# Kernel optimization log

Hardware: AMD Instinct MI355X
Metric: run time of the kernel (lower is better)

Reference implementation:

```python
import jax, jax.numpy as jnp
import numpy as np

D_MODEL = 1024
NUM_HEADS = 16
D_K = D_MODEL // NUM_HEADS
B, T = 2, 2048
NEG = -1e9


def setup_inputs() -> dict:
    key = jax.random.key(0)
    ks = jax.random.split(key, 12)
    s = 1.0 / np.sqrt(D_MODEL)
    q = jax.random.normal(ks[0], (B, T, D_MODEL), jnp.float32)
    k = jax.random.normal(ks[1], (B, T, D_MODEL), jnp.float32)
    v = jax.random.normal(ks[2], (B, T, D_MODEL), jnp.float32)
    # padding mask: True = valid key; realistic per-example lengths
    lengths = jnp.array([T, 3 * T // 4], dtype=jnp.int32)
    key_padding_mask = jnp.arange(T)[None, :] < lengths[:, None]
    Wq = jax.random.uniform(ks[3], (D_MODEL, D_MODEL), jnp.float32, -s, s)
    bq = jax.random.uniform(ks[4], (D_MODEL,), jnp.float32, -s, s)
    Wk = jax.random.uniform(ks[5], (D_MODEL, D_MODEL), jnp.float32, -s, s)
    bk = jax.random.uniform(ks[6], (D_MODEL,), jnp.float32, -s, s)
    Wv = jax.random.uniform(ks[7], (D_MODEL, D_MODEL), jnp.float32, -s, s)
    bv = jax.random.uniform(ks[8], (D_MODEL,), jnp.float32, -s, s)
    Wo = jax.random.uniform(ks[9], (D_MODEL, D_MODEL), jnp.float32, -s, s)
    bo = jax.random.uniform(ks[10], (D_MODEL,), jnp.float32, -s, s)
    return {"q": q, "k": k, "v": v, "key_padding_mask": key_padding_mask,
            "Wq": Wq, "bq": bq, "Wk": Wk, "bk": bk,
            "Wv": Wv, "bv": bv, "Wo": Wo, "bo": bo}


def reference(q, k, v, key_padding_mask, Wq, bq, Wk, bk, Wv, bv, Wo, bo):
    Bq, Tq, D = q.shape
    Tk = k.shape[1]
    # projections (torch Linear: x @ W.T + b), split heads -> [B, H, T, d_k]
    Q = (q @ Wq.T + bq).reshape(Bq, Tq, NUM_HEADS, D_K).transpose(0, 2, 1, 3)
    K = (k @ Wk.T + bk).reshape(Bq, Tk, NUM_HEADS, D_K).transpose(0, 2, 1, 3)
    V = (v @ Wv.T + bv).reshape(Bq, Tk, NUM_HEADS, D_K).transpose(0, 2, 1, 3)
    logits = jnp.einsum("bhqd,bhkd->bhqk", Q, K) / jnp.sqrt(jnp.float32(D_K))
    causal = jnp.tril(jnp.ones((Tq, Tk), dtype=bool))  # [Tq, Tk]
    mask = causal[None, None, :, :] & key_padding_mask[:, None, None, :]
    logits = jnp.where(mask, logits, NEG)
    scores = jax.nn.softmax(logits, axis=-1)
    out = jnp.einsum("bhqk,bhkd->bhqd", scores, V)
    out = out.transpose(0, 2, 1, 3).reshape(Bq, Tq, D)
    # dropout is identity in eval mode
    return out @ Wo.T + bo
```

## Files before the change

### kernel.cpp

```cpp
#include <hip/hip_runtime.h>
#include <stdint.h>

#define D_MODEL 1024
#define NHEAD 16
#define DK 64
#define BATCH 2
#define SEQ 2048
#define NROW 4096

typedef __attribute__((ext_vector_type(8))) _Float16 f16x8;
typedef __attribute__((ext_vector_type(4))) float f32x4;

__device__ __forceinline__ uint16_t f2h(float x) {
    _Float16 h = (_Float16)x;
    union { _Float16 h; uint16_t u; } cv;
    cv.h = h;
    return cv.u;
}

__device__ __forceinline__ float fexp2(float x) {
#if __has_builtin(__builtin_amdgcn_exp2f)
    return __builtin_amdgcn_exp2f(x);
#else
    return exp2f(x);
#endif
}

__device__ __forceinline__ void lds_dma16(const uint16_t* g, uint16_t* l) {
    __builtin_amdgcn_global_load_lds((const __attribute__((address_space(1))) void*)g,
                                     (__attribute__((address_space(3))) void*)l,
                                     16, 0, 0);
}

struct CvtArgs {
    const float* src[7];
    uint16_t* dst[7];
    int n4[7];
};
__global__ void cvt_all_kernel(CvtArgs a, const int* __restrict__ mask, int* __restrict__ lens) {
    int t = blockIdx.y;
    if (t == 7) {
        if (blockIdx.x != 0) return;
        __shared__ int red[256];
        int tid = threadIdx.x;
        int mx = 0;
        for (int i = tid; i < 1024; i += 256) { int v = mask[i]; if (v > mx) mx = v; }
        red[tid] = mx; __syncthreads();
        for (int s = 128; s > 0; s >>= 1) { if (tid < s) { if (red[tid+s] > red[tid]) red[tid] = red[tid+s]; } __syncthreads(); }
        int bytemode = (red[0] > 1);
        __syncthreads();
        const unsigned char* mb = (const unsigned char*)mask;
        for (int b = 0; b < BATCH; ++b) {
            int cnt = 0;
            for (int tt = tid; tt < SEQ; tt += 256) {
                int v = bytemode ? (int)mb[b*SEQ + tt] : mask[b*SEQ + tt];
                cnt += (v != 0) ? 1 : 0;
            }
            red[tid] = cnt; __syncthreads();
            for (int s = 128; s > 0; s >>= 1) { if (tid < s) red[tid] += red[tid+s]; __syncthreads(); }
            if (tid == 0) lens[b] = red[0];
            __syncthreads();
        }
        return;
    }
    const float* src = a.src[t];
    uint16_t* dst = a.dst[t];
    int n4 = a.n4[t];
    int i = blockIdx.x * blockDim.x + threadIdx.x;
    int stride = gridDim.x * blockDim.x;
    for (; i < n4; i += stride) {
        float4 v = ((const float4*)src)[i];
        ushort4 o;
        o.x = f2h(v.x); o.y = f2h(v.y); o.z = f2h(v.z); o.w = f2h(v.w);
        ((ushort4*)dst)[i] = o;
    }
}

__device__ __forceinline__ void gemm_tile_core(const uint16_t* __restrict__ A,
                                               const uint16_t* __restrict__ W,
                                               int bx, int by,
                                               uint16_t* As, uint16_t* Bs,
                                               f32x4 (&acc)[4][4]) {
    const f32x4 fzero = {0.f, 0.f, 0.f, 0.f};
    int tid = threadIdx.x;
    int lane = tid & 63, wave = tid >> 6;
    int wm = wave >> 1, wn = wave & 1;
    int l15 = lane & 15, quad = lane >> 4;
    int rl = lane >> 3, cb8 = lane & 7;
#pragma unroll
    for (int mi = 0; mi < 4; mi++)
#pragma unroll
        for (int ni = 0; ni < 4; ni++) acc[mi][ni] = fzero;

    for (int k0 = 0; k0 < D_MODEL; k0 += 64) {
        __syncthreads();
#pragma unroll
        for (int i = 0; i < 4; ++i) {
            int d8 = wave * 4 + i;
            int row = d8 * 8 + rl;
            int cbg = cb8 ^ rl;
            lds_dma16(A + (size_t)(bx * 128 + row) * D_MODEL + k0 + cbg * 8, As + d8 * 512);
            lds_dma16(W + (size_t)(by * 128 + row) * D_MODEL + k0 + cbg * 8, Bs + d8 * 512);
        }
        __syncthreads();
#pragma unroll
        for (int ks = 0; ks < 2; ks++) {
            f16x8 af[4], bf[4];
#pragma unroll
            for (int mi = 0; mi < 4; mi++) {
                int row = wm * 64 + mi * 16 + l15;
                af[mi] = *(const f16x8*)(As + row * 64 + (((ks * 4 + quad) ^ (row & 7)) * 8));
            }
#pragma unroll
            for (int ni = 0; ni < 4; ni++) {
                int row = wn * 64 + ni * 16 + l15;
                bf[ni] = *(const f16x8*)(Bs + row * 64 + (((ks * 4 + quad) ^ (row & 7)) * 8));
            }
#pragma unroll
            for (int mi = 0; mi < 4; mi++)
#pragma unroll
                for (int ni = 0; ni < 4; ni++)
                    acc[mi][ni] = __builtin_amdgcn_mfma_f32_16x16x32_f16(af[mi], bf[ni], acc[mi][ni], 0, 0, 0);
        }
    }
}

#define TS_STRIDE 136
__global__ __launch_bounds__(256, 3) void qkv_kernel(
    const uint16_t* __restrict__ qb, const uint16_t* __restrict__ kb, const uint16_t* __restrict__ vb,
    const uint16_t* __restrict__ wq, const uint16_t* __restrict__ wk, const uint16_t* __restrict__ wv,
    const float* __restrict__ bq, const float* __restrict__ bk, const float* __restrict__ bv,
    uint16_t* __restrict__ Qh, uint16_t* __restrict__ Kh, uint16_t* __restrict__ Vth) {
    __shared__ uint16_t smem[TS_STRIDE * 128];
    uint16_t* As = smem;
    uint16_t* Bs = smem + 128 * 64;
    int v = blockIdx.z;
    const uint16_t* A = (v == 0) ? qb : ((v == 1) ? kb : vb);
    const uint16_t* W = (v == 0) ? wq : ((v == 1) ? wk : wv);
    const float* bias = (v == 0) ? bq : ((v == 1) ? bk : bv);
    f32x4 acc[4][4];
    gemm_tile_core(A, W, blockIdx.x, blockIdx.y, As, Bs, acc);

    int tid = threadIdx.x, lane = tid & 63, wave = tid >> 6;
    int wm = wave >> 1, wn = wave & 1, l15 = lane & 15, quad = lane >> 4;
    const float QSCALE = 0.125f * 1.44269504088896f;

    if (v == 2) {
        __syncthreads();
        uint16_t* Ts = smem;
#pragma unroll
        for (int mi = 0; mi < 4; mi++) {
#pragma unroll
            for (int ni = 0; ni < 4; ni++) {
                int col = wn * 64 + ni * 16 + l15;
                float bcol = bias[blockIdx.y * 128 + col];
#pragma unroll
                for (int r = 0; r < 4; r++) {
                    int tl = wm * 64 + mi * 16 + quad * 4 + r;
                    Ts[col * TS_STRIDE + tl] = f2h(acc[mi][ni][r] + bcol);
                }
            }
        }
        __syncthreads();
        int col = tid >> 1, th = (tid & 1) << 6;
        int gcol = blockIdx.y * 128 + col;
        int h = gcol >> 6, d = gcol & 63;
        int grow0 = blockIdx.x * 128;
        int b = grow0 >> 11, t = (grow0 & (SEQ - 1)) + th;
        size_t base = (((size_t)(b * NHEAD + h) << 6) + d) * SEQ + t;
#pragma unroll
        for (int j = 0; j < 8; j++)
            *(uint4*)(Vth + base + j * 8) = *(const uint4*)(Ts + col * TS_STRIDE + th + j * 8);
        return;
    }

#pragma unroll
    for (int mi = 0; mi < 4; mi++) {
#pragma unroll
        for (int ni = 0; ni < 4; ni++) {
            int gcol = blockIdx.y * 128 + wn * 64 + ni * 16 + l15;
            float bcol = bias[gcol];
            int h = gcol >> 6, d = gcol & 63;
#pragma unroll
            for (int r = 0; r < 4; r++) {
                int grow = blockIdx.x * 128 + wm * 64 + mi * 16 + quad * 4 + r;
                int b = grow >> 11, t = grow & (SEQ - 1);
                float val = acc[mi][ni][r] + bcol;
                size_t bh = (size_t)(b * NHEAD + h);
                if (v == 0) Qh[(bh * SEQ + t) * 64 + d] = f2h(val * QSCALE);
                else        Kh[(bh * SEQ + t) * 64 + d] = f2h(val);
            }
        }
    }
}

__global__ __launch_bounds__(256, 3) void outproj_kernel(
    const uint16_t* __restrict__ attn, const uint16_t* __restrict__ wo,
    const float* __restrict__ bo, float* __restrict__ out) {
    __shared__ uint16_t As[128 * 64], Bs[128 * 64];
    f32x4 acc[4][4];
    gemm_tile_core(attn, wo, blockIdx.x, blockIdx.y, As, Bs, acc);
    int tid = threadIdx.x, lane = tid & 63, wave = tid >> 6;
    int wm = wave >> 1, wn = wave & 1, l15 = lane & 15, quad = lane >> 4;
#pragma unroll
    for (int mi = 0; mi < 4; mi++) {
#pragma unroll
        for (int ni = 0; ni < 4; ni++) {
            int gcol = blockIdx.y * 128 + wn * 64 + ni * 16 + l15;
            float bcol = bo[gcol];
#pragma unroll
            for (int r = 0; r < 4; r++) {
                int grow = blockIdx.x * 128 + wm * 64 + mi * 16 + quad * 4 + r;
                out[(size_t)grow * D_MODEL + gcol] = acc[mi][ni][r] + bcol;
            }
        }
    }
}

#define PIPE_WAIT2_BARRIER() do { asm volatile("s_waitcnt vmcnt(2)" ::: "memory"); __builtin_amdgcn_s_barrier(); } while (0)
#define PIPE_WAIT0_BARRIER() do { asm volatile("s_waitcnt vmcnt(0)" ::: "memory"); __builtin_amdgcn_s_barrier(); } while (0)

__device__ __forceinline__ void flash_item(
    int qt, int bh, int b, int h, int L,
    const uint16_t* __restrict__ Qh, const uint16_t* __restrict__ Kh, const uint16_t* __restrict__ Vth,
    uint16_t* __restrict__ attn,
    uint16_t* KtA, uint16_t* VtA, uint16_t* Ptw) {
    const f32x4 fzero = {0.f, 0.f, 0.f, 0.f};
    const float MFIX = 6.0f;
    int tid = threadIdx.x, lane = tid & 63, w = tid >> 6;
    int l15 = lane & 15, quad = lane >> 4, l7 = l15 & 7;
    int q0 = qt * 64;
    int rl = lane >> 3, cb8 = lane & 7;

    f16x8 ones;
#pragma unroll
    for (int j = 0; j < 8; j++) ones[j] = (_Float16)1.0f;

    f16x8 qf[2];
#pragma unroll
    for (int ks = 0; ks < 2; ks++)
        qf[ks] = *(const f16x8*)(Qh + ((size_t)bh * SEQ + q0 + w * 16 + l15) * 64 + ks * 32 + quad * 8);

    f32x4 o_acc[4], l_acc = fzero;
#pragma unroll
    for (int ni = 0; ni < 4; ni++) o_acc[ni] = fzero;

    int nkt_p = (L + 63) >> 6;
    int nkt = (qt + 1 < nkt_p) ? (qt + 1) : nkt_p;

    const uint16_t* Kbh = Kh + (size_t)bh * SEQ * 64;
    const uint16_t* Vbh = Vth + ((size_t)bh << 6) * SEQ;

    auto stageK = [&](int kt_, int slot) {
#pragma unroll
        for (int i_ = 0; i_ < 2; ++i_) {
            int d8 = w * 2 + i_;
            int row = d8 * 8 + rl;
            int cbg = cb8 ^ rl;
            lds_dma16(Kbh + (size_t)(kt_ * 64 + row) * 64 + cbg * 8, KtA + slot * 4096 + d8 * 512);
        }
    };
    auto stageV = [&](int kt_, int slot) {
#pragma unroll
        for (int i_ = 0; i_ < 2; ++i_) {
            int d8 = w * 2 + i_;
            int row = d8 * 8 + rl;
            int cbg = cb8 ^ rl;
            lds_dma16(Vbh + (size_t)row * SEQ + kt_ * 64 + cbg * 8, VtA + slot * 4096 + d8 * 512);
        }
    };

    stageV(0, 0);
    stageK(0, 0);
    PIPE_WAIT0_BARRIER();
    stageK((1 < nkt) ? 1 : 0, 1);

    int kcur = 0, vcur = 0;
    for (int kt = 0; kt < nkt; ++kt) {
        int ktV = (kt + 1 < nkt) ? kt + 1 : nkt - 1;
        int ktK = (kt + 2 < nkt) ? kt + 2 : nkt - 1;
        stageV(ktV, (kt + 1) & 1);
        int ks2 = (kcur >= 1) ? kcur - 1 : 2;
        stageK(ktK, ks2);

        const uint16_t* Kc = KtA + kcur * 4096;
        const uint16_t* Vc = VtA + vcur * 4096;

        f32x4 s_acc[4];
#pragma unroll
        for (int ni = 0; ni < 4; ni++) s_acc[ni] = fzero;
#pragma unroll
        for (int ks = 0; ks < 2; ks++) {
            f16x8 kf[4];
#pragma unroll
            for (int ni = 0; ni < 4; ni++) {
                int row = ni * 16 + l15;
                kf[ni] = *(const f16x8*)(Kc + row * 64 + (((ks * 4 + quad) ^ (row & 7)) * 8));
            }
#pragma unroll
            for (int ni = 0; ni < 4; ni++)
                s_acc[ni] = __builtin_amdgcn_mfma_f32_16x16x32_f16(qf[ks], kf[ni], s_acc[ni], 0, 0, 0);
        }

        bool full = (kt < qt) && (kt * 64 + 64 <= L);
#pragma unroll
        for (int r = 0; r < 4; r++) {
            int prow = quad * 4 + r;
            int q_idx = q0 + w * 16 + prow;
            int pr7 = prow & 7;
#pragma unroll
            for (int ni = 0; ni < 4; ni++) {
                float s = s_acc[ni][r];
                if (!full) {
                    int key = kt * 64 + ni * 16 + l15;
                    s = ((key <= q_idx) && (key < L)) ? s : -1e9f;
                }
                float p = fexp2(s - MFIX);
                int cb = ni * 2 + (l15 >> 3);
                Ptw[prow * 64 + ((cb ^ pr7) * 8) + l7] = f2h(p);
            }
        }
        __asm__ __volatile__("" ::: "memory");

#pragma unroll
        for (int ks = 0; ks < 2; ks++) {
            f16x8 pa = *(const f16x8*)(Ptw + l15 * 64 + (((ks * 4 + quad) ^ l7) * 8));
            l_acc = __builtin_amdgcn_mfma_f32_16x16x32_f16(pa, ones, l_acc, 0, 0, 0);
            f16x8 vbf[4];
#pragma unroll
            for (int ni = 0; ni < 4; ni++) {
                int row = ni * 16 + l15;
                vbf[ni] = *(const f16x8*)(Vc + row * 64 + (((ks * 4 + quad) ^ (row & 7)) * 8));
            }
#pragma unroll
            for (int ni = 0; ni < 4; ni++)
                o_acc[ni] = __builtin_amdgcn_mfma_f32_16x16x32_f16(pa, vbf[ni], o_acc[ni], 0, 0, 0);
        }

        PIPE_WAIT2_BARRIER();
        kcur = (kcur == 2) ? 0 : kcur + 1;
        vcur ^= 1;
    }

#pragma unroll
    for (int r = 0; r < 4; r++) {
        float inv = 1.0f / l_acc[r];
        int q_idx = q0 + w * 16 + quad * 4 + r;
#pragma unroll
        for (int ni = 0; ni < 4; ni++) {
            attn[((size_t)(b * SEQ + q_idx)) * D_MODEL + h * 64 + ni * 16 + l15] =
                f2h(o_acc[ni][r] * inv);
        }
    }
}

__global__ __launch_bounds__(256, 3) void attn_kernel(
    const uint16_t* __restrict__ Qh, const uint16_t* __restrict__ Kh, const uint16_t* __restrict__ Vth,
    uint16_t* __restrict__ attn, const int* __restrict__ lens) {
    __shared__ uint16_t Kt[3 * 4096];
    __shared__ uint16_t Vt[2 * 4096];
    __shared__ uint16_t Pt[4 * 1024];
    int n = (int)blockIdx.x;
    int xcd = n & 7;
    int i = n >> 3;
    int j = (xcd << 2) | (i & 3);
    int bh = ((j & 1) << 4) | (j >> 1);
    int x = i >> 2;
    int b = bh >> 4, h = bh & 15;
    int L = lens[b];
    int w = threadIdx.x >> 6;
    uint16_t* Ptw = Pt + w * 1024;
    flash_item(31 - x, bh, b, h, L, Qh, Kh, Vth, attn, Kt, Vt, Ptw);
    flash_item(x, bh, b, h, L, Qh, Kh, Vth, attn, Kt, Vt, Ptw);
}

extern "C" void kernel_launch(void* const* d_in, const int* in_sizes, int n_in,
                              void* d_out, int out_size, void* d_ws, size_t ws_size,
                              hipStream_t stream) {
    const float* q  = (const float*)d_in[0];
    const float* k  = (const float*)d_in[1];
    const float* v  = (const float*)d_in[2];
    const int*   mask = (const int*)d_in[3];
    const float* Wq = (const float*)d_in[4];
    const float* bq = (const float*)d_in[5];
    const float* Wk = (const float*)d_in[6];
    const float* bk = (const float*)d_in[7];
    const float* Wv = (const float*)d_in[8];
    const float* bv = (const float*)d_in[9];
    const float* Wo = (const float*)d_in[10];
    const float* bo = (const float*)d_in[11];
    float* out = (float*)d_out;

    char* ws = (char*)d_ws;
    size_t off = 0;
    auto alloc = [&](size_t bytes) -> char* {
        char* p = ws + off;
        off += (bytes + 255) & ~(size_t)255;
        return p;
    };
    const size_t inp_e = (size_t)NROW * D_MODEL;
    const size_t w_e   = (size_t)D_MODEL * D_MODEL;
    uint16_t* qbf  = (uint16_t*)alloc(inp_e * 2);
    uint16_t* kbf  = (uint16_t*)alloc(inp_e * 2);
    uint16_t* vbf  = (uint16_t*)alloc(inp_e * 2);
    uint16_t* wqb  = (uint16_t*)alloc(w_e * 2);
    uint16_t* wkb  = (uint16_t*)alloc(w_e * 2);
    uint16_t* wvb  = (uint16_t*)alloc(w_e * 2);
    uint16_t* wob  = (uint16_t*)alloc(w_e * 2);
    uint16_t* Qhb  = (uint16_t*)alloc(inp_e * 2);
    uint16_t* Khb  = (uint16_t*)alloc(inp_e * 2);
    uint16_t* Vtb  = (uint16_t*)alloc(inp_e * 2);
    uint16_t* attb = (uint16_t*)alloc(inp_e * 2);
    int* lens      = (int*)alloc(256);

    CvtArgs ca;
    ca.src[0] = q;  ca.dst[0] = qbf; ca.n4[0] = (int)(inp_e / 4);
    ca.src[1] = k;  ca.dst[1] = kbf; ca.n4[1] = (int)(inp_e / 4);
    ca.src[2] = v;  ca.dst[2] = vbf; ca.n4[2] = (int)(inp_e / 4);
    ca.src[3] = Wq; ca.dst[3] = wqb; ca.n4[3] = (int)(w_e / 4);
    ca.src[4] = Wk; ca.dst[4] = wkb; ca.n4[4] = (int)(w_e / 4);
    ca.src[5] = Wv; ca.dst[5] = wvb; ca.n4[5] = (int)(w_e / 4);
    ca.src[6] = Wo; ca.dst[6] = wob; ca.n4[6] = (int)(w_e / 4);
    cvt_all_kernel<<<dim3(128, 8), 256, 0, stream>>>(ca, mask, lens);

    qkv_kernel<<<dim3(32, 8, 3), 256, 0, stream>>>(qbf, kbf, vbf, wqb, wkb, wvb,
                                                   bq, bk, bv, Qhb, Khb, Vtb);
    attn_kernel<<<dim3(512, 1), 256, 0, stream>>>(Qhb, Khb, Vtb, attb, lens);
    outproj_kernel<<<dim3(32, 8), 256, 0, stream>>>(attb, wob, bo, out);
}
```

Before: 227.6 us.

## Process paired causal query tiles in one pass sharing K/V tile loads

Each block now processes its two query tiles (a long one, 31-x, and a short one, x) together in a single KV loop rather than two sequential loops. The short tile reuses each staged K/V tile while it is active, which cuts repeated global-to-LDS staging and pipeline restarts. The change also adds s_setprio around the MFMA sections, doubles the P scratch, and reorders block-to-tile mapping. In exchange, register use rises and occupancy is dropped from 3 to 2 blocks per CU.

```diff
diff --git a/kernel.cpp b/kernel.cpp
--- a/kernel.cpp
+++ b/kernel.cpp
@@ -220,33 +220,36 @@
 #define PIPE_WAIT2_BARRIER() do { asm volatile("s_waitcnt vmcnt(2)" ::: "memory"); __builtin_amdgcn_s_barrier(); } while (0)
 #define PIPE_WAIT0_BARRIER() do { asm volatile("s_waitcnt vmcnt(0)" ::: "memory"); __builtin_amdgcn_s_barrier(); } while (0)
 
-__device__ __forceinline__ void flash_item(
-    int qt, int bh, int b, int h, int L,
+__device__ __forceinline__ void flash_pair(
+    int qtA, int qtB, int bh, int b, int h, int L,
     const uint16_t* __restrict__ Qh, const uint16_t* __restrict__ Kh, const uint16_t* __restrict__ Vth,
     uint16_t* __restrict__ attn,
-    uint16_t* KtA, uint16_t* VtA, uint16_t* Ptw) {
+    uint16_t* KtA, uint16_t* VtA, uint16_t* PtwA, uint16_t* PtwB) {
     const f32x4 fzero = {0.f, 0.f, 0.f, 0.f};
     const float MFIX = 6.0f;
     int tid = threadIdx.x, lane = tid & 63, w = tid >> 6;
     int l15 = lane & 15, quad = lane >> 4, l7 = l15 & 7;
-    int q0 = qt * 64;
+    int q0A = qtA * 64, q0B = qtB * 64;
     int rl = lane >> 3, cb8 = lane & 7;
 
     f16x8 ones;
 #pragma unroll
     for (int j = 0; j < 8; j++) ones[j] = (_Float16)1.0f;
 
-    f16x8 qf[2];
-#pragma unroll
-    for (int ks = 0; ks < 2; ks++)
-        qf[ks] = *(const f16x8*)(Qh + ((size_t)bh * SEQ + q0 + w * 16 + l15) * 64 + ks * 32 + quad * 8);
-
-    f32x4 o_acc[4], l_acc = fzero;
-#pragma unroll
-    for (int ni = 0; ni < 4; ni++) o_acc[ni] = fzero;
+    f16x8 qfA[2], qfB[2];
+#pragma unroll
+    for (int ks = 0; ks < 2; ks++) {
+        qfA[ks] = *(const f16x8*)(Qh + ((size_t)bh * SEQ + q0A + w * 16 + l15) * 64 + ks * 32 + quad * 8);
+        qfB[ks] = *(const f16x8*)(Qh + ((size_t)bh * SEQ + q0B + w * 16 + l15) * 64 + ks * 32 + quad * 8);
+    }
+
+    f32x4 oA[4], oB[4], lAcc = fzero, lBcc = fzero;
+#pragma unroll
+    for (int ni = 0; ni < 4; ni++) { oA[ni] = fzero; oB[ni] = fzero; }
 
     int nkt_p = (L + 63) >> 6;
-    int nkt = (qt + 1 < nkt_p) ? (qt + 1) : nkt_p;
+    int nktA = (qtA + 1 < nkt_p) ? (qtA + 1) : nkt_p;
+    int nktB = (qtB + 1 < nkt_p) ? (qtB + 1) : nkt_p;
 
     const uint16_t* Kbh = Kh + (size_t)bh * SEQ * 64;
     const uint16_t* Vbh = Vth + ((size_t)bh << 6) * SEQ;
@@ -273,22 +276,24 @@
     stageV(0, 0);
     stageK(0, 0);
     PIPE_WAIT0_BARRIER();
-    stageK((1 < nkt) ? 1 : 0, 1);
+    stageK((1 < nktA) ? 1 : 0, 1);
 
     int kcur = 0, vcur = 0;
-    for (int kt = 0; kt < nkt; ++kt) {
-        int ktV = (kt + 1 < nkt) ? kt + 1 : nkt - 1;
-        int ktK = (kt + 2 < nkt) ? kt + 2 : nkt - 1;
+    for (int kt = 0; kt < nktA; ++kt) {
+        int ktV = (kt + 1 < nktA) ? kt + 1 : nktA - 1;
+        int ktK = (kt + 2 < nktA) ? kt + 2 : nktA - 1;
         stageV(ktV, (kt + 1) & 1);
         int ks2 = (kcur >= 1) ? kcur - 1 : 2;
         stageK(ktK, ks2);
 
         const uint16_t* Kc = KtA + kcur * 4096;
         const uint16_t* Vc = VtA + vcur * 4096;
-
-        f32x4 s_acc[4];
-#pragma unroll
-        for (int ni = 0; ni < 4; ni++) s_acc[ni] = fzero;
+        bool actB = (kt < nktB);
+
+        f32x4 sA[4], sB[4];
+#pragma unroll
+        for (int ni = 0; ni < 4; ni++) { sA[ni] = fzero; sB[ni] = fzero; }
+        __builtin_amdgcn_s_setprio(1);
 #pragma unroll
         for (int ks = 0; ks < 2; ks++) {
             f16x8 kf[4];
@@ -299,33 +304,67 @@
             }
 #pragma unroll
             for (int ni = 0; ni < 4; ni++)
-                s_acc[ni] = __builtin_amdgcn_mfma_f32_16x16x32_f16(qf[ks], kf[ni], s_acc[ni], 0, 0, 0);
-        }
-
-        bool full = (kt < qt) && (kt * 64 + 64 <= L);
-#pragma unroll
-        for (int r = 0; r < 4; r++) {
-            int prow = quad * 4 + r;
-            int q_idx = q0 + w * 16 + prow;
-            int pr7 = prow & 7;
-#pragma unroll
-            for (int ni = 0; ni < 4; ni++) {
-                float s = s_acc[ni][r];
-                if (!full) {
-                    int key = kt * 64 + ni * 16 + l15;
-                    s = ((key <= q_idx) && (key < L)) ? s : -1e9f;
+                sA[ni] = __builtin_amdgcn_mfma_f32_16x16x32_f16(qfA[ks], kf[ni], sA[ni], 0, 0, 0);
+            if (actB) {
+#pragma unroll
+                for (int ni = 0; ni < 4; ni++)
+                    sB[ni] = __builtin_amdgcn_mfma_f32_16x16x32_f16(qfB[ks], kf[ni], sB[ni], 0, 0, 0);
+            }
+        }
+        __builtin_amdgcn_s_setprio(0);
+
+        {
+            bool fullA = (kt < qtA) && (kt * 64 + 64 <= L);
+#pragma unroll
+            for (int r = 0; r < 4; r++) {
+                int prow = quad * 4 + r;
+                int q_idx = q0A + w * 16 + prow;
+                int pr7 = prow & 7;
+#pragma unroll
+                for (int ni = 0; ni < 4; ni++) {
+                    float s = sA[ni][r];
+                    if (!fullA) {
+                        int key = kt * 64 + ni * 16 + l15;
+                        s = ((key <= q_idx) && (key < L)) ? s : -1e9f;
+                    }
+                    float p = fexp2(s - MFIX);
+                    int cb = ni * 2 + (l15 >> 3);
+                    PtwA[prow * 64 + ((cb ^ pr7) * 8) + l7] = f2h(p);
                 }
-                float p = fexp2(s - MFIX);
-                int cb = ni * 2 + (l15 >> 3);
-                Ptw[prow * 64 + ((cb ^ pr7) * 8) + l7] = f2h(p);
+            }
+        }
+        if (actB) {
+            bool fullB = (kt < qtB) && (kt * 64 + 64 <= L);
+#pragma unroll
+            for (int r = 0; r < 4; r++) {
+                int prow = quad * 4 + r;
+                int q_idx = q0B + w * 16 + prow;
+                int pr7 = prow & 7;
+#pragma unroll
+                for (int ni = 0; ni < 4; ni++) {
+                    float s = sB[ni][r];
+                    if (!fullB) {
+                        int key = kt * 64 + ni * 16 + l15;
+                        s = ((key <= q_idx) && (key < L)) ? s : -1e9f;
+                    }
+                    float p = fexp2(s - MFIX);
+                    int cb = ni * 2 + (l15 >> 3);
+                    PtwB[prow * 64 + ((cb ^ pr7) * 8) + l7] = f2h(p);
+                }
             }
         }
         __asm__ __volatile__("" ::: "memory");
 
+        __builtin_amdgcn_s_setprio(1);
 #pragma unroll
         for (int ks = 0; ks < 2; ks++) {
-            f16x8 pa = *(const f16x8*)(Ptw + l15 * 64 + (((ks * 4 + quad) ^ l7) * 8));
-            l_acc = __builtin_amdgcn_mfma_f32_16x16x32_f16(pa, ones, l_acc, 0, 0, 0);
+            f16x8 paA = *(const f16x8*)(PtwA + l15 * 64 + (((ks * 4 + quad) ^ l7) * 8));
+            lAcc = __builtin_amdgcn_mfma_f32_16x16x32_f16(paA, ones, lAcc, 0, 0, 0);
+            f16x8 paB;
+            if (actB) {
+                paB = *(const f16x8*)(PtwB + l15 * 64 + (((ks * 4 + quad) ^ l7) * 8));
+                lBcc = __builtin_amdgcn_mfma_f32_16x16x32_f16(paB, ones, lBcc, 0, 0, 0);
+            }
             f16x8 vbf[4];
 #pragma unroll
             for (int ni = 0; ni < 4; ni++) {
@@ -334,8 +373,14 @@
             }
 #pragma unroll
             for (int ni = 0; ni < 4; ni++)
-                o_acc[ni] = __builtin_amdgcn_mfma_f32_16x16x32_f16(pa, vbf[ni], o_acc[ni], 0, 0, 0);
-        }
+                oA[ni] = __builtin_amdgcn_mfma_f32_16x16x32_f16(paA, vbf[ni], oA[ni], 0, 0, 0);
+            if (actB) {
+#pragma unroll
+                for (int ni = 0; ni < 4; ni++)
+                    oB[ni] = __builtin_amdgcn_mfma_f32_16x16x32_f16(paB, vbf[ni], oB[ni], 0, 0, 0);
+            }
+        }
+        __builtin_amdgcn_s_setprio(0);
 
         PIPE_WAIT2_BARRIER();
         kcur = (kcur == 2) ? 0 : kcur + 1;
@@ -344,34 +389,46 @@
 
 #pragma unroll
     for (int r = 0; r < 4; r++) {
-        float inv = 1.0f / l_acc[r];
-        int q_idx = q0 + w * 16 + quad * 4 + r;
+        float inv = 1.0f / lAcc[r];
+        int q_idx = q0A + w * 16 + quad * 4 + r;
 #pragma unroll
         for (int ni = 0; ni < 4; ni++) {
             attn[((size_t)(b * SEQ + q_idx)) * D_MODEL + h * 64 + ni * 16 + l15] =
-                f2h(o_acc[ni][r] * inv);
-        }
-    }
-}
-
-__global__ __launch_bounds__(256, 3) void attn_kernel(
+                f2h(oA[ni][r] * inv);
+        }
+    }
+#pragma unroll
+    for (int r = 0; r < 4; r++) {
+        float inv = 1.0f / lBcc[r];
+        int q_idx = q0B + w * 16 + quad * 4 + r;
+#pragma unroll
+        for (int ni = 0; ni < 4; ni++) {
+            attn[((size_t)(b * SEQ + q_idx)) * D_MODEL + h * 64 + ni * 16 + l15] =
+                f2h(oB[ni][r] * inv);
+        }
+    }
+}
+
+__global__ __launch_bounds__(256, 2) void attn_kernel(
     const uint16_t* __restrict__ Qh, const uint16_t* __restrict__ Kh, const uint16_t* __restrict__ Vth,
     uint16_t* __restrict__ attn, const int* __restrict__ lens) {
     __shared__ uint16_t Kt[3 * 4096];
     __shared__ uint16_t Vt[2 * 4096];
-    __shared__ uint16_t Pt[4 * 1024];
+    __shared__ uint16_t Pt[8 * 1024];
     int n = (int)blockIdx.x;
     int xcd = n & 7;
     int i = n >> 3;
-    int j = (xcd << 2) | (i & 3);
-    int bh = ((j & 1) << 4) | (j >> 1);
-    int x = i >> 2;
+    int hs = i & 3;
+    int j = i >> 2;
+    int x = (j < 8) ? j : (23 - j);
+    int jj = (xcd << 2) | hs;
+    int bh = ((jj & 1) << 4) | (jj >> 1);
     int b = bh >> 4, h = bh & 15;
     int L = lens[b];
     int w = threadIdx.x >> 6;
-    uint16_t* Ptw = Pt + w * 1024;
-    flash_item(31 - x, bh, b, h, L, Qh, Kh, Vth, attn, Kt, Vt, Ptw);
-    flash_item(x, bh, b, h, L, Qh, Kh, Vth, attn, Kt, Vt, Ptw);
+    uint16_t* PtwA = Pt + w * 2048;
+    uint16_t* PtwB = PtwA + 1024;
+    flash_pair(31 - x, x, bh, b, h, L, Qh, Kh, Vth, attn, Kt, Vt, PtwA, PtwB);
 }
 
 extern "C" void kernel_launch(void* const* d_in, const int* in_sizes, int n_in,
```

Result: slower. 235.2 us (+3.3%).

## Load K/V fragments directly from global memory, dropping LDS staging pipeline

Applied to the files above, without the earlier changes.

The attention kernel no longer stages K and V tiles into shared memory through async LDS DMA with a triple/double-buffered pipeline and barriers. Each wave now reads its MFMA K and V fragments straight from global memory into registers at the start of every key tile, so the block-wide barriers and most of the LDS footprint go away. The cost is that the four waves each fetch the same K/V data redundantly through L1/L2, with no prefetch overlap across iterations. Launch bounds are lowered from 3 to 2 blocks per SM to leave room for the extra registers.

```diff
diff --git a/kernel.cpp b/kernel.cpp
--- a/kernel.cpp
+++ b/kernel.cpp
@@ -217,20 +217,15 @@
     }
 }
 
-#define PIPE_WAIT2_BARRIER() do { asm volatile("s_waitcnt vmcnt(2)" ::: "memory"); __builtin_amdgcn_s_barrier(); } while (0)
-#define PIPE_WAIT0_BARRIER() do { asm volatile("s_waitcnt vmcnt(0)" ::: "memory"); __builtin_amdgcn_s_barrier(); } while (0)
-
 __device__ __forceinline__ void flash_item(
     int qt, int bh, int b, int h, int L,
     const uint16_t* __restrict__ Qh, const uint16_t* __restrict__ Kh, const uint16_t* __restrict__ Vth,
-    uint16_t* __restrict__ attn,
-    uint16_t* KtA, uint16_t* VtA, uint16_t* Ptw) {
+    uint16_t* __restrict__ attn, uint16_t* Ptw) {
     const f32x4 fzero = {0.f, 0.f, 0.f, 0.f};
     const float MFIX = 6.0f;
     int tid = threadIdx.x, lane = tid & 63, w = tid >> 6;
     int l15 = lane & 15, quad = lane >> 4, l7 = l15 & 7;
     int q0 = qt * 64;
-    int rl = lane >> 3, cb8 = lane & 7;
 
     f16x8 ones;
 #pragma unroll
@@ -248,59 +243,34 @@
     int nkt_p = (L + 63) >> 6;
     int nkt = (qt + 1 < nkt_p) ? (qt + 1) : nkt_p;
 
-    const uint16_t* Kbh = Kh + (size_t)bh * SEQ * 64;
+    const uint16_t* kb = Kh + (size_t)bh * SEQ * 64 + l15 * 64 + quad * 8;
     const uint16_t* Vbh = Vth + ((size_t)bh << 6) * SEQ;
-
-    auto stageK = [&](int kt_, int slot) {
-#pragma unroll
-        for (int i_ = 0; i_ < 2; ++i_) {
-            int d8 = w * 2 + i_;
-            int row = d8 * 8 + rl;
-            int cbg = cb8 ^ rl;
-            lds_dma16(Kbh + (size_t)(kt_ * 64 + row) * 64 + cbg * 8, KtA + slot * 4096 + d8 * 512);
-        }
-    };
-    auto stageV = [&](int kt_, int slot) {
-#pragma unroll
-        for (int i_ = 0; i_ < 2; ++i_) {
-            int d8 = w * 2 + i_;
-            int row = d8 * 8 + rl;
-            int cbg = cb8 ^ rl;
-            lds_dma16(Vbh + (size_t)row * SEQ + kt_ * 64 + cbg * 8, VtA + slot * 4096 + d8 * 512);
-        }
-    };
-
-    stageV(0, 0);
-    stageK(0, 0);
-    PIPE_WAIT0_BARRIER();
-    stageK((1 < nkt) ? 1 : 0, 1);
-
-    int kcur = 0, vcur = 0;
+    const uint16_t* vb0 = Vbh + (size_t)(l15) * SEQ + quad * 8;
+    const uint16_t* vb1 = Vbh + (size_t)(16 + l15) * SEQ + quad * 8;
+    const uint16_t* vb2 = Vbh + (size_t)(32 + l15) * SEQ + quad * 8;
+    const uint16_t* vb3 = Vbh + (size_t)(48 + l15) * SEQ + quad * 8;
+
     for (int kt = 0; kt < nkt; ++kt) {
-        int ktV = (kt + 1 < nkt) ? kt + 1 : nkt - 1;
-        int ktK = (kt + 2 < nkt) ? kt + 2 : nkt - 1;
-        stageV(ktV, (kt + 1) & 1);
-        int ks2 = (kcur >= 1) ? kcur - 1 : 2;
-        stageK(ktK, ks2);
-
-        const uint16_t* Kc = KtA + kcur * 4096;
-        const uint16_t* Vc = VtA + vcur * 4096;
+        f16x8 kf[2][4], vf[2][4];
+#pragma unroll
+        for (int ks = 0; ks < 2; ks++) {
+#pragma unroll
+            for (int ni = 0; ni < 4; ni++)
+                kf[ks][ni] = *(const f16x8*)(kb + kt * 4096 + ni * 1024 + ks * 32);
+            vf[ks][0] = *(const f16x8*)(vb0 + kt * 64 + ks * 32);
+            vf[ks][1] = *(const f16x8*)(vb1 + kt * 64 + ks * 32);
+            vf[ks][2] = *(const f16x8*)(vb2 + kt * 64 + ks * 32);
+            vf[ks][3] = *(const f16x8*)(vb3 + kt * 64 + ks * 32);
+        }
 
         f32x4 s_acc[4];
 #pragma unroll
         for (int ni = 0; ni < 4; ni++) s_acc[ni] = fzero;
 #pragma unroll
-        for (int ks = 0; ks < 2; ks++) {
-            f16x8 kf[4];
-#pragma unroll
-            for (int ni = 0; ni < 4; ni++) {
-                int row = ni * 16 + l15;
-                kf[ni] = *(const f16x8*)(Kc + row * 64 + (((ks * 4 + quad) ^ (row & 7)) * 8));
-            }
+        for (int ks = 0; ks < 2; ks++)
 #pragma unroll
             for (int ni = 0; ni < 4; ni++)
-                s_acc[ni] = __builtin_amdgcn_mfma_f32_16x16x32_f16(qf[ks], kf[ni], s_acc[ni], 0, 0, 0);
-        }
+                s_acc[ni] = __builtin_amdgcn_mfma_f32_16x16x32_f16(qf[ks], kf[ks][ni], s_acc[ni], 0, 0, 0);
 
         bool full = (kt < qt) && (kt * 64 + 64 <= L);
 #pragma unroll
@@ -326,20 +296,11 @@
         for (int ks = 0; ks < 2; ks++) {
             f16x8 pa = *(const f16x8*)(Ptw + l15 * 64 + (((ks * 4 + quad) ^ l7) * 8));
             l_acc = __builtin_amdgcn_mfma_f32_16x16x32_f16(pa, ones, l_acc, 0, 0, 0);
-            f16x8 vbf[4];
-#pragma unroll
-            for (int ni = 0; ni < 4; ni++) {
-                int row = ni * 16 + l15;
-                vbf[ni] = *(const f16x8*)(Vc + row * 64 + (((ks * 4 + quad) ^ (row & 7)) * 8));
-            }
 #pragma unroll
             for (int ni = 0; ni < 4; ni++)
-                o_acc[ni] = __builtin_amdgcn_mfma_f32_16x16x32_f16(pa, vbf[ni], o_acc[ni], 0, 0, 0);
-        }
-
-        PIPE_WAIT2_BARRIER();
-        kcur = (kcur == 2) ? 0 : kcur + 1;
-        vcur ^= 1;
+                o_acc[ni] = __builtin_amdgcn_mfma_f32_16x16x32_f16(pa, vf[ks][ni], o_acc[ni], 0, 0, 0);
+        }
+        __asm__ __volatile__("" ::: "memory");
     }
 
 #pragma unroll
@@ -354,11 +315,9 @@
     }
 }
 
-__global__ __launch_bounds__(256, 3) void attn_kernel(
+__global__ __launch_bounds__(256, 2) void attn_kernel(
     const uint16_t* __restrict__ Qh, const uint16_t* __restrict__ Kh, const uint16_t* __restrict__ Vth,
     uint16_t* __restrict__ attn, const int* __restrict__ lens) {
-    __shared__ uint16_t Kt[3 * 4096];
-    __shared__ uint16_t Vt[2 * 4096];
     __shared__ uint16_t Pt[4 * 1024];
     int n = (int)blockIdx.x;
     int xcd = n & 7;
@@ -370,8 +329,8 @@
     int L = lens[b];
     int w = threadIdx.x >> 6;
     uint16_t* Ptw = Pt + w * 1024;
-    flash_item(31 - x, bh, b, h, L, Qh, Kh, Vth, attn, Kt, Vt, Ptw);
-    flash_item(x, bh, b, h, L, Qh, Kh, Vth, attn, Kt, Vt, Ptw);
+    flash_item(31 - x, bh, b, h, L, Qh, Kh, Vth, attn, Ptw);
+    flash_item(x, bh, b, h, L, Qh, Kh, Vth, attn, Ptw);
 }
 
 extern "C" void kernel_launch(void* const* d_in, const int* in_sizes, int n_in,
```

Result: slower. 309.9 us (+36.2%).
